# Optimization experiments

Hardware: AMD Instinct MI355X
Metric: run time of the kernel (lower is better)

The kernel has to match this reference:

```python
import jax, jax.numpy as jnp
import numpy as np

DIM = 1024
N_SLOTS = 64
SCALE = 1.0 / np.sqrt(DIM).astype(np.float32)


def _orthogonal(key, n, scale):
    a = jax.random.normal(key, (n, n), dtype=jnp.float32)
    q, r = jnp.linalg.qr(a)
    q = q * jnp.sign(jnp.diag(r))[None, :]
    return q * scale


def setup_inputs() -> dict:
    key = jax.random.key(0)
    ks = jax.random.split(key, 8)
    B, T, D = 16, 1024, DIM
    s = 1.0 / np.sqrt(D)
    x = jax.random.normal(ks[0], (B, T, D), dtype=jnp.float32)
    in_proj_w = jax.random.uniform(ks[1], (D, D), minval=-s, maxval=s, dtype=jnp.float32)
    out_proj_w = jax.random.uniform(ks[2], (D, D), minval=-s, maxval=s, dtype=jnp.float32)
    gate_proj_w = jax.random.uniform(ks[3], (D, D), minval=-s, maxval=s, dtype=jnp.float32)
    W_x = jax.random.uniform(ks[4], (D, D), minval=-s, maxval=s, dtype=jnp.float32)
    W_h = _orthogonal(ks[5], D, 0.9)
    W_write = jax.random.uniform(ks[6], (D, D), minval=-s, maxval=s, dtype=jnp.float32)
    b_h = jnp.zeros((D,), dtype=jnp.float32)
    return {"x": x, "in_proj_w": in_proj_w, "out_proj_w": out_proj_w,
            "gate_proj_w": gate_proj_w, "W_x": W_x, "W_h": W_h,
            "W_write": W_write, "b_h": b_h}


def _cell(x_proj, W_x, W_h, W_write, b_h):
    # x_proj: [B, T, D]
    B, T, D = x_proj.shape
    wx_all = jnp.einsum('btd,ed->bte', x_proj, W_x)  # precomputed W_x @ x
    h_tape0 = jnp.zeros((B, N_SLOTS, D), dtype=x_proj.dtype)
    h_work0 = jnp.zeros((B, D), dtype=x_proj.dtype)

    def step(carry, wx_t):
        h_tape, h_work = carry
        Rh = h_work @ W_h.T
        read_attn = jax.nn.softmax(jnp.einsum('bd,bnd->bn', h_work, h_tape) * SCALE, axis=-1)
        read = jnp.einsum('bn,bnd->bd', read_attn, h_tape)
        h_work = jnp.tanh(Rh + wx_t + read + b_h)
        write_val = h_work @ W_write.T
        write_attn = jax.nn.softmax(jnp.einsum('bd,bnd->bn', h_work, h_tape) * SCALE, axis=-1)
        wa = write_attn[..., None]  # [B, N, 1]
        h_tape = (1.0 - wa) * h_tape + wa * write_val[:, None, :]
        return (h_tape, h_work), h_work

    (h_tape_f, h_work_f), h_work_all = jax.lax.scan(
        step, (h_tape0, h_work0), jnp.swapaxes(wx_all, 0, 1))
    return jnp.swapaxes(h_work_all, 0, 1), h_tape_f, h_work_f


def reference(x, in_proj_w, out_proj_w, gate_proj_w, W_x, W_h, W_write, b_h):
    x_proj = x @ in_proj_w.T  # [B, T, D]
    h_work_all, h_tape_f, h_work_f = _cell(x_proj, W_x, W_h, W_write, b_h)
    gate = jax.nn.silu(x @ gate_proj_w.T)
    output = (h_work_all * gate) @ out_proj_w.T
    return output, h_tape_f, h_work_f
```

## Files before the change

kernel.cpp:

```cpp
#include <hip/hip_runtime.h>
#include <math.h>

#define SCALE_F 0.03125f

template<bool BT, int EPI>
__global__ __launch_bounds__(256) void gemm_nt(const float* __restrict__ A,
                                               const float* __restrict__ Bm,
                                               float* __restrict__ C,
                                               int M, int N, int K) {
  __shared__ float As[32][68];
  __shared__ float Bs[32][68];
  const int tid = threadIdx.x;
  const int n0 = blockIdx.x * 64;
  const int m0 = blockIdx.y * 64;
  const int i0 = (tid >> 4) * 4;
  const int j0 = (tid & 15) * 4;
  float acc[4][4] = {};

  for (int k0 = 0; k0 < K; k0 += 32) {
#pragma unroll
    for (int s = 0; s < 2; ++s) {
      int id = tid + 256 * s;
      int r = id >> 3, c4 = id & 7;
      float4 v = *(const float4*)&A[(size_t)(m0 + r) * K + k0 + c4 * 4];
      As[c4 * 4 + 0][r] = v.x; As[c4 * 4 + 1][r] = v.y;
      As[c4 * 4 + 2][r] = v.z; As[c4 * 4 + 3][r] = v.w;
    }
    if (BT) {
#pragma unroll
      for (int s = 0; s < 2; ++s) {
        int id = tid + 256 * s;
        int r = id >> 3, c4 = id & 7;
        float4 v = *(const float4*)&Bm[(size_t)(n0 + r) * K + k0 + c4 * 4];
        Bs[c4 * 4 + 0][r] = v.x; Bs[c4 * 4 + 1][r] = v.y;
        Bs[c4 * 4 + 2][r] = v.z; Bs[c4 * 4 + 3][r] = v.w;
      }
    } else {
#pragma unroll
      for (int s = 0; s < 2; ++s) {
        int id = tid + 256 * s;
        int kk = id >> 4, c4 = id & 15;
        float4 v = *(const float4*)&Bm[(size_t)(k0 + kk) * N + n0 + c4 * 4];
        *(float4*)&Bs[kk][c4 * 4] = v;
      }
    }
    __syncthreads();
#pragma unroll
    for (int kk = 0; kk < 32; ++kk) {
      float4 a = *(const float4*)&As[kk][i0];
      float4 b = *(const float4*)&Bs[kk][j0];
      float av[4] = {a.x, a.y, a.z, a.w};
      float bv[4] = {b.x, b.y, b.z, b.w};
#pragma unroll
      for (int ii = 0; ii < 4; ++ii)
#pragma unroll
        for (int jj = 0; jj < 4; ++jj)
          acc[ii][jj] = fmaf(av[ii], bv[jj], acc[ii][jj]);
    }
    __syncthreads();
  }

#pragma unroll
  for (int ii = 0; ii < 4; ++ii) {
    float4 v;
    float* vp = (float*)&v;
#pragma unroll
    for (int jj = 0; jj < 4; ++jj) {
      float x = acc[ii][jj];
      if (EPI == 1) x = x / (1.0f + __expf(-x));
      vp[jj] = x;
    }
    *(float4*)&C[(size_t)(m0 + i0 + ii) * N + n0 + j0] = v;
  }
}

typedef unsigned long long u64;
__device__ __forceinline__ u64 ald64(const u64* p) {
  return __hip_atomic_load(p, __ATOMIC_RELAXED, __HIP_MEMORY_SCOPE_AGENT);
}
__device__ __forceinline__ void ast64(u64* p, u64 v) {
  __hip_atomic_store(p, v, __ATOMIC_RELAXED, __HIP_MEMORY_SCOPE_AGENT);
}
__device__ __forceinline__ u64 pk(float v, int j) {
  return ((u64)(unsigned)j << 32) | (u64)__float_as_uint(v);
}
__device__ __forceinline__ float lo(u64 u) {
  return __uint_as_float((unsigned)u);
}
__device__ __forceinline__ float pollv(const u64* p, int j) {
  u64 u = ald64(p);
  while ((unsigned)(u >> 32) != (unsigned)j) {
    __builtin_amdgcn_s_sleep(1);
    u = ald64(p);
  }
  return lo(u);
}

#define TIDX(n, e) ((n) * 64 + (((e) + (n)) & 63))

#define REP32(M) M(0) M(1) M(2) M(3) M(4) M(5) M(6) M(7) M(8) M(9) M(10) \
  M(11) M(12) M(13) M(14) M(15) M(16) M(17) M(18) M(19) M(20) M(21) M(22) \
  M(23) M(24) M(25) M(26) M(27) M(28) M(29) M(30) M(31)

#define RW(i) const float wh##i = Whp[32 * (i)]; \
              const float ww##i = Wwp[32 * (i)];
#define MVI(i) { float4 hh = ht4[cseg + 32 * (i)]; \
  ah0 = fmaf(wh##i, hh.x, ah0); ah1 = fmaf(wh##i, hh.y, ah1); \
  ah2 = fmaf(wh##i, hh.z, ah2); ah3 = fmaf(wh##i, hh.w, ah3); \
  aw0 = fmaf(ww##i, hh.x, aw0); aw1 = fmaf(ww##i, hh.y, aw1); \
  aw2 = fmaf(ww##i, hh.z, aw2); aw3 = fmaf(ww##i, hh.w, aw3); }

#define TAGOK(u) ((unsigned)((u) >> 32) == tj)

__global__ __launch_bounds__(512) void scan_kernel(
    const float* __restrict__ W_h, const float* __restrict__ W_wr,
    const float* __restrict__ b_h, const float* __restrict__ gate,
    float* __restrict__ wx,
    u64* __restrict__ h2,
    u64* __restrict__ ps2,
    u64* __restrict__ Rh2,
    u64* __restrict__ wv2,
    u64* __restrict__ qp2b,
    float* __restrict__ hfin,
    float* __restrict__ tape_out)
{
  const int tid  = threadIdx.x;
  const int wg   = blockIdx.x;
  const int g    = wg >> 6;
  const int idx  = wg & 63;
  const int b_loc = idx >> 4;
  const int es   = idx & 15;
  const int gb   = g * 4;
  const int bsel = gb + b_loc;
  const int E0   = es * 64;
  const int R0   = es * 64 + b_loc * 16;
  const int w    = tid >> 6;
  const int lane = tid & 63;
  const int row  = tid >> 5;
  const int cseg = tid & 31;
  const int gr   = R0 + row;
  const int nwr  = tid >> 3;
  const int ksb  = tid & 7;

  __shared__ float h_t[4096];
  __shared__ float tape_l[4096];
  __shared__ float ws_lds[64], wa_lds[64], attn_lds[64];
  __shared__ float wv_lds[64], Rh_lds[64], h_own[64], read_lds[64];
  __shared__ volatile float lds_pad[12288];
  lds_pad[tid] = 0.0f; lds_pad[tid + 512] = 0.0f;

  const float* Whp = W_h + (size_t)gr * 1024 + cseg;
  const float* Wwp = W_wr + (size_t)gr * 1024 + cseg;
  REP32(RW)

  const float4* ht4 = (const float4*)h_t;

  for (int i = tid; i < 4096; i += 512) tape_l[i] = 0.0f;

  float bh_r = 0.0f;
  if (w == 0) bh_r = b_h[E0 + lane];
  __syncthreads();

  if (w == 0) {
    size_t xi = (size_t)bsel * 1048576 + E0 + lane;
    float hv = tanhf(wx[xi] + bh_r);
    h_own[lane] = hv;
    ast64(&h2[(size_t)bsel * 1024 + E0 + lane], pk(hv, 1));
    wx[xi] = hv * gate[xi];
  }
  if (tid < 64) ast64(&ps2[(size_t)bsel * 1024 + es * 64 + tid], pk(0.0f, 1));
  __syncthreads();

  for (int j = 1; j <= 1024; ++j) {
    const bool last = (j == 1024);
    const unsigned tj = (unsigned)j;

    float p0, p1;
    {
      const int d0 = tid, d1 = tid + 512;
      const u64* hp = &h2[(size_t)gb * 1024];
      const u64* pA = &ps2[(size_t)bsel * 1024 + (ksb * 2) * 64 + nwr];
      const u64* pB = &ps2[(size_t)bsel * 1024 + (ksb * 2 + 1) * 64 + nwr];
      u64 a0, a1, a2, a3, c0, c1, c2, c3, u0, u1;
      for (;;) {
        a0 = ald64(hp + 0 * 1024 + d0); a1 = ald64(hp + 1 * 1024 + d0);
        a2 = ald64(hp + 2 * 1024 + d0); a3 = ald64(hp + 3 * 1024 + d0);
        c0 = ald64(hp + 0 * 1024 + d1); c1 = ald64(hp + 1 * 1024 + d1);
        c2 = ald64(hp + 2 * 1024 + d1); c3 = ald64(hp + 3 * 1024 + d1);
        u0 = ald64(pA); u1 = ald64(pB);
        if (TAGOK(a0) && TAGOK(a1) && TAGOK(a2) && TAGOK(a3) &&
            TAGOK(c0) && TAGOK(c1) && TAGOK(c2) && TAGOK(c3) &&
            TAGOK(u0) && TAGOK(u1)) break;
        __builtin_amdgcn_s_sleep(1);
      }
      ((float4*)h_t)[d0] = make_float4(lo(a0), lo(a1), lo(a2), lo(a3));
      ((float4*)h_t)[d1] = make_float4(lo(c0), lo(c1), lo(c2), lo(c3));
      p0 = lo(u0); p1 = lo(u1);
    }
    float wxv = 0.0f, gv = 0.0f;
    size_t xj = 0;
    if (w == 0 && !last) {
      xj  = (size_t)bsel * 1048576 + (size_t)j * 1024 + E0 + lane;
      wxv = wx[xj];
      gv  = gate[xj];
    }
    __syncthreads();

    {
      float s = p0 + p1;
      s += __shfl_xor(s, 1);
      s += __shfl_xor(s, 2);
      s += __shfl_xor(s, 4);
      if (ksb == 0) ws_lds[nwr] = s;
    }
    float ah0 = 0.0f, ah1 = 0.0f, ah2 = 0.0f, ah3 = 0.0f;
    float aw0 = 0.0f, aw1 = 0.0f, aw2 = 0.0f, aw3 = 0.0f;
    REP32(MVI)
#pragma unroll
    for (int m = 1; m < 32; m <<= 1) {
      ah0 += __shfl_xor(ah0, m); ah1 += __shfl_xor(ah1, m);
      ah2 += __shfl_xor(ah2, m); ah3 += __shfl_xor(ah3, m);
      aw0 += __shfl_xor(aw0, m); aw1 += __shfl_xor(aw1, m);
      aw2 += __shfl_xor(aw2, m); aw3 += __shfl_xor(aw3, m);
    }
    {
      float4 hrow = ht4[gr];
      float t0 = aw0 * hrow.x, t1 = aw1 * hrow.y;
      float t2 = aw2 * hrow.z, t3 = aw3 * hrow.w;
      t0 += __shfl_xor(t0, 32); t1 += __shfl_xor(t1, 32);
      t2 += __shfl_xor(t2, 32); t3 += __shfl_xor(t3, 32);
      if (lane == 0) {
        ast64(&qp2b[(size_t)(gb + 0) * 512 + idx * 8 + w], pk(t0, j));
        ast64(&qp2b[(size_t)(gb + 1) * 512 + idx * 8 + w], pk(t1, j));
        ast64(&qp2b[(size_t)(gb + 2) * 512 + idx * 8 + w], pk(t2, j));
        ast64(&qp2b[(size_t)(gb + 3) * 512 + idx * 8 + w], pk(t3, j));
      }
    }
    if (cseg == 0) {
      ast64(&Rh2[(size_t)(gb + 0) * 1024 + gr], pk(ah0, j));
      ast64(&Rh2[(size_t)(gb + 1) * 1024 + gr], pk(ah1, j));
      ast64(&Rh2[(size_t)(gb + 2) * 1024 + gr], pk(ah2, j));
      ast64(&Rh2[(size_t)(gb + 3) * 1024 + gr], pk(ah3, j));
      ast64(&wv2[(size_t)(gb + 0) * 1024 + gr], pk(aw0, j));
      ast64(&wv2[(size_t)(gb + 1) * 1024 + gr], pk(aw1, j));
      ast64(&wv2[(size_t)(gb + 2) * 1024 + gr], pk(aw2, j));
      ast64(&wv2[(size_t)(gb + 3) * 1024 + gr], pk(aw3, j));
    }
    __syncthreads();

    if (w == 0) {
      float s = ws_lds[lane] * SCALE_F;
      float m = s;
#pragma unroll
      for (int off = 1; off < 64; off <<= 1) m = fmaxf(m, __shfl_xor(m, off));
      float ex = __expf(s - m);
      float sum = ex;
#pragma unroll
      for (int off = 1; off < 64; off <<= 1) sum += __shfl_xor(sum, off);
      wa_lds[lane] = ex / sum;
    } else if (w == 1) {
      if (!last) {
        const u64* qb = &qp2b[(size_t)bsel * 512 + lane * 8];
        u64 q0, q1, q2, q3, q4, q5, q6, q7;
        for (;;) {
          q0 = ald64(qb + 0); q1 = ald64(qb + 1); q2 = ald64(qb + 2);
          q3 = ald64(qb + 3); q4 = ald64(qb + 4); q5 = ald64(qb + 5);
          q6 = ald64(qb + 6); q7 = ald64(qb + 7);
          if (TAGOK(q0) && TAGOK(q1) && TAGOK(q2) && TAGOK(q3) &&
              TAGOK(q4) && TAGOK(q5) && TAGOK(q6) && TAGOK(q7)) break;
          __builtin_amdgcn_s_sleep(1);
        }
        float qv = lo(q0) + lo(q1) + lo(q2) + lo(q3) +
                   lo(q4) + lo(q5) + lo(q6) + lo(q7);
#pragma unroll
        for (int off = 1; off < 64; off <<= 1) qv += __shfl_xor(qv, off);
        float wsr = ws_lds[lane];
        float sm = wsr * SCALE_F;
        float m = sm;
#pragma unroll
        for (int off = 1; off < 64; off <<= 1) m = fmaxf(m, __shfl_xor(m, off));
        float ex = __expf(sm - m);
        float sum = ex;
#pragma unroll
        for (int off = 1; off < 64; off <<= 1) sum += __shfl_xor(sum, off);
        float wa_l = ex / sum;
        float rs = fmaf(wa_l, qv - wsr, wsr) * SCALE_F;
        float m2 = rs;
#pragma unroll
        for (int off = 1; off < 64; off <<= 1) m2 = fmaxf(m2, __shfl_xor(m2, off));
        float ex2 = __expf(rs - m2);
        float sum2 = ex2;
#pragma unroll
        for (int off = 1; off < 64; off <<= 1) sum2 += __shfl_xor(sum2, off);
        attn_lds[lane] = ex2 / sum2;
      }
    } else if (w == 2) {
      wv_lds[lane] = pollv(&wv2[(size_t)bsel * 1024 + E0 + lane], j);
    } else if (w == 3) {
      Rh_lds[lane] = pollv(&Rh2[(size_t)bsel * 1024 + E0 + lane], j);
    }
    __syncthreads();

    {
      float wa = wa_lds[nwr];
#pragma unroll
      for (int i = 0; i < 8; ++i) {
        int e = ksb * 8 + i;
        int ix = TIDX(nwr, e);
        float t = tape_l[ix];
        tape_l[ix] = fmaf(wa, wv_lds[e] - t, t);
      }
    }
    if (last) break;
    __syncthreads();

    {
      int ge = tid >> 3, gn = tid & 7;
      float gsum = 0.0f;
#pragma unroll
      for (int i = 0; i < 8; ++i) {
        int n = gn * 8 + i;
        gsum = fmaf(attn_lds[n], tape_l[TIDX(n, ge)], gsum);
      }
      gsum += __shfl_xor(gsum, 1);
      gsum += __shfl_xor(gsum, 2);
      gsum += __shfl_xor(gsum, 4);
      if (gn == 0) read_lds[ge] = gsum;
    }
    __syncthreads();

    if (w == 0) {
      float hv = tanhf(Rh_lds[lane] + wxv + read_lds[lane] + bh_r);
      h_own[lane] = hv;
      ast64(&h2[(size_t)bsel * 1024 + E0 + lane], pk(hv, j + 1));
      wx[xj] = hv * gv;
    }
    __syncthreads();

    {
      float s = 0.0f;
#pragma unroll
      for (int i = 0; i < 8; ++i) {
        int e = ksb * 8 + i;
        s = fmaf(h_own[e], tape_l[TIDX(nwr, e)], s);
      }
      s += __shfl_xor(s, 1);
      s += __shfl_xor(s, 2);
      s += __shfl_xor(s, 4);
      if (ksb == 0) ast64(&ps2[(size_t)bsel * 1024 + es * 64 + nwr], pk(s, j + 1));
    }
  }

#pragma unroll
  for (int i = 0; i < 8; ++i) {
    int e = ksb * 8 + i;
    tape_out[(size_t)(bsel * 64 + nwr) * 1024 + E0 + e] = tape_l[TIDX(nwr, e)];
  }
  if (w == 0) hfin[(size_t)bsel * 1024 + E0 + lane] = h_own[lane];
}

extern "C" void kernel_launch(void* const* d_in, const int* in_sizes, int n_in,
                              void* d_out, int out_size, void* d_ws, size_t ws_size,
                              hipStream_t stream) {
  (void)in_sizes; (void)n_in; (void)out_size; (void)ws_size;
  const float* x      = (const float*)d_in[0];
  const float* in_w   = (const float*)d_in[1];
  const float* out_w  = (const float*)d_in[2];
  const float* gate_w = (const float*)d_in[3];
  const float* W_x    = (const float*)d_in[4];
  const float* W_h    = (const float*)d_in[5];
  const float* W_wr   = (const float*)d_in[6];
  const float* b_h    = (const float*)d_in[7];

  float* out  = (float*)d_out;
  float* tape = out + (size_t)16 * 1024 * 1024;
  float* hfin = tape + (size_t)16 * 64 * 1024;

  float* ws = (float*)d_ws;
  u64* h2   = (u64*)ws;
  u64* ps2  = (u64*)(ws + 32768);
  u64* Rh2  = (u64*)(ws + 65536);
  u64* wv2  = (u64*)(ws + 98304);
  u64* qp2b = (u64*)(ws + 131072);
  float* M1 = ws;
  float* wx = ws + (1 << 20);

  float* gate = out;

  dim3 blk(256);
  gemm_nt<false, 0><<<dim3(16, 16), blk, 0, stream>>>(W_x, in_w, M1, 1024, 1024, 1024);
  gemm_nt<true, 1><<<dim3(16, 256), blk, 0, stream>>>(x, gate_w, gate, 16384, 1024, 1024);
  gemm_nt<true, 0><<<dim3(16, 256), blk, 0, stream>>>(x, M1, wx, 16384, 1024, 1024);
  hipMemsetAsync(ws, 0, 147456 * sizeof(float), stream);
  scan_kernel<<<256, 512, 0, stream>>>(W_h, W_wr, b_h, gate, wx, h2, ps2,
                                       Rh2, wv2, qp2b, hfin, tape);
  gemm_nt<true, 0><<<dim3(16, 256), blk, 0, stream>>>(wx, out_w, out, 16384, 1024, 1024);
}
```

Baseline: 12.69 ms.

## Replace per-value tagged polling with per-workgroup flags and restructure step schedule

Values exchanged between workgroups are no longer packed with a 64-bit step tag. They are now plain floats guarded by per-workgroup step flags (fA for h, fB for Rh/wv/qp) that one wave polls with __all. The read computation is rewritten to use the pre-update tape plus a correction term (s2*write_val), so h can be computed and published before the tape update, shortening the critical path of each step. This halves the bytes moved for exchanged data and removes one barrier, but adds flag publish latency and an explicit vmcnt wait before each flag store.

```diff
diff --git a/kernel.cpp b/kernel.cpp
--- a/kernel.cpp
+++ b/kernel.cpp
@@ -75,6 +75,18 @@
 }
 
 typedef unsigned long long u64;
+__device__ __forceinline__ float ald(const float* p) {
+  return __hip_atomic_load(p, __ATOMIC_RELAXED, __HIP_MEMORY_SCOPE_AGENT);
+}
+__device__ __forceinline__ void ast(float* p, float v) {
+  __hip_atomic_store(p, v, __ATOMIC_RELAXED, __HIP_MEMORY_SCOPE_AGENT);
+}
+__device__ __forceinline__ int ildi(const int* p) {
+  return __hip_atomic_load(p, __ATOMIC_RELAXED, __HIP_MEMORY_SCOPE_AGENT);
+}
+__device__ __forceinline__ void iast(int* p, int v) {
+  __hip_atomic_store(p, v, __ATOMIC_RELAXED, __HIP_MEMORY_SCOPE_AGENT);
+}
 __device__ __forceinline__ u64 ald64(const u64* p) {
   return __hip_atomic_load(p, __ATOMIC_RELAXED, __HIP_MEMORY_SCOPE_AGENT);
 }
@@ -84,8 +96,9 @@
 __device__ __forceinline__ u64 pk(float v, int j) {
   return ((u64)(unsigned)j << 32) | (u64)__float_as_uint(v);
 }
-__device__ __forceinline__ float lo(u64 u) {
-  return __uint_as_float((unsigned)u);
+__device__ __forceinline__ float lo(u64 u) { return __uint_as_float((unsigned)u); }
+__device__ __forceinline__ float hi(u64 u) {
+  return __uint_as_float((unsigned)(u >> 32));
 }
 __device__ __forceinline__ float pollv(const u64* p, int j) {
   u64 u = ald64(p);
@@ -110,17 +123,16 @@
   aw0 = fmaf(ww##i, hh.x, aw0); aw1 = fmaf(ww##i, hh.y, aw1); \
   aw2 = fmaf(ww##i, hh.z, aw2); aw3 = fmaf(ww##i, hh.w, aw3); }
 
-#define TAGOK(u) ((unsigned)((u) >> 32) == tj)
-
 __global__ __launch_bounds__(512) void scan_kernel(
     const float* __restrict__ W_h, const float* __restrict__ W_wr,
     const float* __restrict__ b_h, const float* __restrict__ gate,
     float* __restrict__ wx,
-    u64* __restrict__ h2,
-    u64* __restrict__ ps2,
-    u64* __restrict__ Rh2,
-    u64* __restrict__ wv2,
-    u64* __restrict__ qp2b,
+    float* __restrict__ hbuf,
+    u64* __restrict__ psb,
+    float* __restrict__ Rhb,
+    float* __restrict__ wvb,
+    float* __restrict__ qpb,
+    int* __restrict__ flags,
     float* __restrict__ hfin,
     float* __restrict__ tape_out)
 {
@@ -146,8 +158,12 @@
   __shared__ float tape_l[4096];
   __shared__ float ws_lds[64], wa_lds[64], attn_lds[64];
   __shared__ float wv_lds[64], Rh_lds[64], h_own[64], read_lds[64];
+  __shared__ float s2_lds;
   __shared__ volatile float lds_pad[12288];
   lds_pad[tid] = 0.0f; lds_pad[tid + 512] = 0.0f;
+
+  int* fA = flags;
+  int* fB = flags + 256;
 
   const float* Whp = W_h + (size_t)gr * 1024 + cseg;
   const float* Wwp = W_wr + (size_t)gr * 1024 + cseg;
@@ -165,38 +181,16 @@
     size_t xi = (size_t)bsel * 1048576 + E0 + lane;
     float hv = tanhf(wx[xi] + bh_r);
     h_own[lane] = hv;
-    ast64(&h2[(size_t)bsel * 1024 + E0 + lane], pk(hv, 1));
+    ast(&hbuf[(size_t)bsel * 1024 + E0 + lane], hv);
     wx[xi] = hv * gate[xi];
   }
-  if (tid < 64) ast64(&ps2[(size_t)bsel * 1024 + es * 64 + tid], pk(0.0f, 1));
+  if (tid < 64) ast64(&psb[(size_t)bsel * 1024 + es * 64 + tid], pk(0.0f, 1));
   __syncthreads();
+  if (tid == 0) iast(&fA[wg], 1);
 
   for (int j = 1; j <= 1024; ++j) {
     const bool last = (j == 1024);
-    const unsigned tj = (unsigned)j;
-
-    float p0, p1;
-    {
-      const int d0 = tid, d1 = tid + 512;
-      const u64* hp = &h2[(size_t)gb * 1024];
-      const u64* pA = &ps2[(size_t)bsel * 1024 + (ksb * 2) * 64 + nwr];
-      const u64* pB = &ps2[(size_t)bsel * 1024 + (ksb * 2 + 1) * 64 + nwr];
-      u64 a0, a1, a2, a3, c0, c1, c2, c3, u0, u1;
-      for (;;) {
-        a0 = ald64(hp + 0 * 1024 + d0); a1 = ald64(hp + 1 * 1024 + d0);
-        a2 = ald64(hp + 2 * 1024 + d0); a3 = ald64(hp + 3 * 1024 + d0);
-        c0 = ald64(hp + 0 * 1024 + d1); c1 = ald64(hp + 1 * 1024 + d1);
-        c2 = ald64(hp + 2 * 1024 + d1); c3 = ald64(hp + 3 * 1024 + d1);
-        u0 = ald64(pA); u1 = ald64(pB);
-        if (TAGOK(a0) && TAGOK(a1) && TAGOK(a2) && TAGOK(a3) &&
-            TAGOK(c0) && TAGOK(c1) && TAGOK(c2) && TAGOK(c3) &&
-            TAGOK(u0) && TAGOK(u1)) break;
-        __builtin_amdgcn_s_sleep(1);
-      }
-      ((float4*)h_t)[d0] = make_float4(lo(a0), lo(a1), lo(a2), lo(a3));
-      ((float4*)h_t)[d1] = make_float4(lo(c0), lo(c1), lo(c2), lo(c3));
-      p0 = lo(u0); p1 = lo(u1);
-    }
+
     float wxv = 0.0f, gv = 0.0f;
     size_t xj = 0;
     if (w == 0 && !last) {
@@ -204,6 +198,25 @@
       wxv = wx[xj];
       gv  = gate[xj];
     }
+    {
+      const int* f = &fA[g * 64];
+      for (;;) {
+        int v = ildi(&f[lane]);
+        if (__all(v >= j)) break;
+        __builtin_amdgcn_s_sleep(1);
+      }
+    }
+
+    {
+      u64 v0 = ald64((const u64*)hbuf + (size_t)(gb + 0) * 512 + tid);
+      u64 v1 = ald64((const u64*)hbuf + (size_t)(gb + 1) * 512 + tid);
+      u64 v2 = ald64((const u64*)hbuf + (size_t)(gb + 2) * 512 + tid);
+      u64 v3 = ald64((const u64*)hbuf + (size_t)(gb + 3) * 512 + tid);
+      ((float4*)h_t)[2 * tid]     = make_float4(lo(v0), lo(v1), lo(v2), lo(v3));
+      ((float4*)h_t)[2 * tid + 1] = make_float4(hi(v0), hi(v1), hi(v2), hi(v3));
+    }
+    float p0 = pollv(&psb[(size_t)bsel * 1024 + (ksb * 2) * 64 + nwr], j);
+    float p1 = pollv(&psb[(size_t)bsel * 1024 + (ksb * 2 + 1) * 64 + nwr], j);
     __syncthreads();
 
     {
@@ -230,23 +243,24 @@
       t0 += __shfl_xor(t0, 32); t1 += __shfl_xor(t1, 32);
       t2 += __shfl_xor(t2, 32); t3 += __shfl_xor(t3, 32);
       if (lane == 0) {
-        ast64(&qp2b[(size_t)(gb + 0) * 512 + idx * 8 + w], pk(t0, j));
-        ast64(&qp2b[(size_t)(gb + 1) * 512 + idx * 8 + w], pk(t1, j));
-        ast64(&qp2b[(size_t)(gb + 2) * 512 + idx * 8 + w], pk(t2, j));
-        ast64(&qp2b[(size_t)(gb + 3) * 512 + idx * 8 + w], pk(t3, j));
+        ast(&qpb[(size_t)(gb + 0) * 512 + idx * 8 + w], t0);
+        ast(&qpb[(size_t)(gb + 1) * 512 + idx * 8 + w], t1);
+        ast(&qpb[(size_t)(gb + 2) * 512 + idx * 8 + w], t2);
+        ast(&qpb[(size_t)(gb + 3) * 512 + idx * 8 + w], t3);
       }
     }
     if (cseg == 0) {
-      ast64(&Rh2[(size_t)(gb + 0) * 1024 + gr], pk(ah0, j));
-      ast64(&Rh2[(size_t)(gb + 1) * 1024 + gr], pk(ah1, j));
-      ast64(&Rh2[(size_t)(gb + 2) * 1024 + gr], pk(ah2, j));
-      ast64(&Rh2[(size_t)(gb + 3) * 1024 + gr], pk(ah3, j));
-      ast64(&wv2[(size_t)(gb + 0) * 1024 + gr], pk(aw0, j));
-      ast64(&wv2[(size_t)(gb + 1) * 1024 + gr], pk(aw1, j));
-      ast64(&wv2[(size_t)(gb + 2) * 1024 + gr], pk(aw2, j));
-      ast64(&wv2[(size_t)(gb + 3) * 1024 + gr], pk(aw3, j));
-    }
-    __syncthreads();
+      ast(&Rhb[(size_t)(gb + 0) * 1024 + gr], ah0);
+      ast(&Rhb[(size_t)(gb + 1) * 1024 + gr], ah1);
+      ast(&Rhb[(size_t)(gb + 2) * 1024 + gr], ah2);
+      ast(&Rhb[(size_t)(gb + 3) * 1024 + gr], ah3);
+      ast(&wvb[(size_t)(gb + 0) * 1024 + gr], aw0);
+      ast(&wvb[(size_t)(gb + 1) * 1024 + gr], aw1);
+      ast(&wvb[(size_t)(gb + 2) * 1024 + gr], aw2);
+      ast(&wvb[(size_t)(gb + 3) * 1024 + gr], aw3);
+    }
+    __syncthreads();
+    if (tid == 0) iast(&fB[wg], j);
 
     if (w == 0) {
       float s = ws_lds[lane] * SCALE_F;
@@ -260,20 +274,6 @@
       wa_lds[lane] = ex / sum;
     } else if (w == 1) {
       if (!last) {
-        const u64* qb = &qp2b[(size_t)bsel * 512 + lane * 8];
-        u64 q0, q1, q2, q3, q4, q5, q6, q7;
-        for (;;) {
-          q0 = ald64(qb + 0); q1 = ald64(qb + 1); q2 = ald64(qb + 2);
-          q3 = ald64(qb + 3); q4 = ald64(qb + 4); q5 = ald64(qb + 5);
-          q6 = ald64(qb + 6); q7 = ald64(qb + 7);
-          if (TAGOK(q0) && TAGOK(q1) && TAGOK(q2) && TAGOK(q3) &&
-              TAGOK(q4) && TAGOK(q5) && TAGOK(q6) && TAGOK(q7)) break;
-          __builtin_amdgcn_s_sleep(1);
-        }
-        float qv = lo(q0) + lo(q1) + lo(q2) + lo(q3) +
-                   lo(q4) + lo(q5) + lo(q6) + lo(q7);
-#pragma unroll
-        for (int off = 1; off < 64; off <<= 1) qv += __shfl_xor(qv, off);
         float wsr = ws_lds[lane];
         float sm = wsr * SCALE_F;
         float m = sm;
@@ -284,6 +284,17 @@
 #pragma unroll
         for (int off = 1; off < 64; off <<= 1) sum += __shfl_xor(sum, off);
         float wa_l = ex / sum;
+        const int* f = &fB[g * 64];
+        for (;;) {
+          int v = ildi(&f[lane]);
+          if (__all(v >= j)) break;
+          __builtin_amdgcn_s_sleep(1);
+        }
+        const float* qb = &qpb[(size_t)bsel * 512 + lane * 8];
+        float qv = ald(qb + 0) + ald(qb + 1) + ald(qb + 2) + ald(qb + 3) +
+                   ald(qb + 4) + ald(qb + 5) + ald(qb + 6) + ald(qb + 7);
+#pragma unroll
+        for (int off = 1; off < 64; off <<= 1) qv += __shfl_xor(qv, off);
         float rs = fmaf(wa_l, qv - wsr, wsr) * SCALE_F;
         float m2 = rs;
 #pragma unroll
@@ -292,15 +303,55 @@
         float sum2 = ex2;
 #pragma unroll
         for (int off = 1; off < 64; off <<= 1) sum2 += __shfl_xor(sum2, off);
-        attn_lds[lane] = ex2 / sum2;
+        float att = ex2 / sum2;
+        attn_lds[lane] = att * (1.0f - wa_l);
+        float s2 = att * wa_l;
+#pragma unroll
+        for (int off = 1; off < 64; off <<= 1) s2 += __shfl_xor(s2, off);
+        if (lane == 0) s2_lds = s2;
       }
     } else if (w == 2) {
-      wv_lds[lane] = pollv(&wv2[(size_t)bsel * 1024 + E0 + lane], j);
+      const int* f = &fB[g * 64];
+      for (;;) {
+        int v = ildi(&f[lane]);
+        if (__all(v >= j)) break;
+        __builtin_amdgcn_s_sleep(1);
+      }
+      wv_lds[lane] = ald(&wvb[(size_t)bsel * 1024 + E0 + lane]);
     } else if (w == 3) {
-      Rh_lds[lane] = pollv(&Rh2[(size_t)bsel * 1024 + E0 + lane], j);
-    }
-    __syncthreads();
-
+      const int* f = &fB[g * 64];
+      for (;;) {
+        int v = ildi(&f[lane]);
+        if (__all(v >= j)) break;
+        __builtin_amdgcn_s_sleep(1);
+      }
+      Rh_lds[lane] = ald(&Rhb[(size_t)bsel * 1024 + E0 + lane]);
+    }
+    __syncthreads();
+
+    if (!last) {
+      int ge = tid >> 3, gn = tid & 7;
+      float gsum = 0.0f;
+#pragma unroll
+      for (int i = 0; i < 8; ++i) {
+        int n = gn * 8 + i;
+        gsum = fmaf(attn_lds[n], tape_l[TIDX(n, ge)], gsum);
+      }
+      gsum += __shfl_xor(gsum, 1);
+      gsum += __shfl_xor(gsum, 2);
+      gsum += __shfl_xor(gsum, 4);
+      if (gn == 0) read_lds[ge] = gsum + s2_lds * wv_lds[ge];
+    }
+    __syncthreads();
+
+    if (w == 0 && !last) {
+      float hv = tanhf(Rh_lds[lane] + wxv + read_lds[lane] + bh_r);
+      h_own[lane] = hv;
+      ast(&hbuf[(size_t)bsel * 1024 + E0 + lane], hv);
+      wx[xj] = hv * gv;
+      asm volatile("s_waitcnt vmcnt(0)" ::: "memory");
+      if (lane == 0) iast(&fA[wg], j + 1);
+    }
     {
       float wa = wa_lds[nwr];
 #pragma unroll
@@ -311,30 +362,7 @@
         tape_l[ix] = fmaf(wa, wv_lds[e] - t, t);
       }
     }
-    if (last) break;
-    __syncthreads();
-
-    {
-      int ge = tid >> 3, gn = tid & 7;
-      float gsum = 0.0f;
-#pragma unroll
-      for (int i = 0; i < 8; ++i) {
-        int n = gn * 8 + i;
-        gsum = fmaf(attn_lds[n], tape_l[TIDX(n, ge)], gsum);
-      }
-      gsum += __shfl_xor(gsum, 1);
-      gsum += __shfl_xor(gsum, 2);
-      gsum += __shfl_xor(gsum, 4);
-      if (gn == 0) read_lds[ge] = gsum;
-    }
-    __syncthreads();
-
-    if (w == 0) {
-      float hv = tanhf(Rh_lds[lane] + wxv + read_lds[lane] + bh_r);
-      h_own[lane] = hv;
-      ast64(&h2[(size_t)bsel * 1024 + E0 + lane], pk(hv, j + 1));
-      wx[xj] = hv * gv;
-    }
+    if (last) { __syncthreads(); break; }
     __syncthreads();
 
     {
@@ -347,7 +375,8 @@
       s += __shfl_xor(s, 1);
       s += __shfl_xor(s, 2);
       s += __shfl_xor(s, 4);
-      if (ksb == 0) ast64(&ps2[(size_t)bsel * 1024 + es * 64 + nwr], pk(s, j + 1));
+      if (ksb == 0)
+        ast64(&psb[(size_t)bsel * 1024 + es * 64 + nwr], pk(s, j + 1));
     }
   }
 
@@ -377,13 +406,14 @@
   float* hfin = tape + (size_t)16 * 64 * 1024;
 
   float* ws = (float*)d_ws;
-  u64* h2   = (u64*)ws;
-  u64* ps2  = (u64*)(ws + 32768);
-  u64* Rh2  = (u64*)(ws + 65536);
-  u64* wv2  = (u64*)(ws + 98304);
-  u64* qp2b = (u64*)(ws + 131072);
-  float* M1 = ws;
-  float* wx = ws + (1 << 20);
+  float* hbuf = ws;
+  u64*   psb  = (u64*)(ws + 16384);
+  float* Rhb  = ws + 49152;
+  float* wvb  = ws + 65536;
+  float* qpb  = ws + 81920;
+  int*   flg  = (int*)(ws + 90112);
+  float* M1   = ws;
+  float* wx   = ws + (1 << 20);
 
   float* gate = out;
 
@@ -391,8 +421,8 @@
   gemm_nt<false, 0><<<dim3(16, 16), blk, 0, stream>>>(W_x, in_w, M1, 1024, 1024, 1024);
   gemm_nt<true, 1><<<dim3(16, 256), blk, 0, stream>>>(x, gate_w, gate, 16384, 1024, 1024);
   gemm_nt<true, 0><<<dim3(16, 256), blk, 0, stream>>>(x, M1, wx, 16384, 1024, 1024);
-  hipMemsetAsync(ws, 0, 147456 * sizeof(float), stream);
-  scan_kernel<<<256, 512, 0, stream>>>(W_h, W_wr, b_h, gate, wx, h2, ps2,
-                                       Rh2, wv2, qp2b, hfin, tape);
+  hipMemsetAsync(ws, 0, 90624 * sizeof(float), stream);
+  scan_kernel<<<256, 512, 0, stream>>>(W_h, W_wr, b_h, gate, wx, hbuf, psb,
+                                       Rhb, wvb, qpb, flg, hfin, tape);
   gemm_nt<true, 0><<<dim3(16, 256), blk, 0, stream>>>(wx, out_w, out, 16384, 1024, 1024);
 }
```

New measurement: 11.16 ms. 1.14x faster.
